# Performance work log

Hardware: AMD Instinct MI355X
Metric: run time of the kernel (lower is better)

The kernel has to match this reference:

```python
import jax, jax.numpy as jnp
import numpy as np


def gcn_conv(x, W, b, src, dst, n_nodes):
    """PyG-style GCNConv: x' = D^{-1/2}(A+I)D^{-1/2} X W + b, with self-loops added."""
    h = x @ W  # [N, F_out]
    # add self-loops
    loop = jnp.arange(n_nodes, dtype=src.dtype)
    s = jnp.concatenate([src, loop])  # [E+N]
    d = jnp.concatenate([dst, loop])  # [E+N]
    # symmetric normalization: deg counted over incoming edges (incl. self-loops)
    deg = jax.ops.segment_sum(jnp.ones_like(d, dtype=h.dtype), d, num_segments=n_nodes)
    dinv = jnp.where(deg > 0, jax.lax.rsqrt(deg), 0.0)
    coef = dinv[s] * dinv[d]  # [E+N]
    msg = h[s] * coef[:, None]  # gather + scale, [E+N, F_out]
    out = jax.ops.segment_sum(msg, d, num_segments=n_nodes)  # scatter-add
    return out + b


def setup_inputs() -> dict:
    key = jax.random.key(0)
    ks = jax.random.split(key, 6)
    N, E, F_IN, F_HID, F_OUT = 50000, 800000, 128, 128, 64
    x = jax.random.normal(ks[0], (N, F_IN), dtype=jnp.float32)
    edge_index = jax.random.randint(ks[1], (2, E), 0, N, dtype=jnp.int64)
    W0 = jax.random.normal(ks[2], (F_IN, F_HID), dtype=jnp.float32) * (F_IN ** -0.5)
    b0 = jnp.zeros((F_HID,), dtype=jnp.float32)
    W1 = jax.random.normal(ks[3], (F_HID, F_HID), dtype=jnp.float32) * (F_HID ** -0.5)
    b1 = jnp.zeros((F_HID,), dtype=jnp.float32)
    W2 = jax.random.normal(ks[4], (F_HID, F_OUT), dtype=jnp.float32) * (F_HID ** -0.5)
    b2 = jnp.zeros((F_OUT,), dtype=jnp.float32)
    return {"x": x, "edge_index": edge_index, "W0": W0, "b0": b0,
            "W1": W1, "b1": b1, "W2": W2, "b2": b2}


def reference(x, edge_index, W0, b0, W1, b1, W2, b2):
    n_nodes = x.shape[0]
    src, dst = edge_index[0], edge_index[1]
    # hidden GCNConv layers with relu (dropout is identity in eval mode)
    h = jax.nn.relu(gcn_conv(x, W0, b0, src, dst, n_nodes))
    h = jax.nn.relu(gcn_conv(h, W1, b1, src, dst, n_nodes))
    # final conv, no activation
    return gcn_conv(h, W2, b2, src, dst, n_nodes)
```

## Files before the change

### kernel.cpp

```cpp
#include <hip/hip_runtime.h>
#include <hip/hip_fp16.h>
#include <type_traits>

#define F_IN 128
#define NPART 8

typedef _Float16 f16x8 __attribute__((ext_vector_type(8)));
typedef _Float16 f16x4 __attribute__((ext_vector_type(4)));
typedef _Float16 f16x2 __attribute__((ext_vector_type(2)));
typedef float f32x4 __attribute__((ext_vector_type(4)));


__global__ void setup_kernel(const float* __restrict__ W0, const float* __restrict__ W1,
                             const float* __restrict__ W2, __half* __restrict__ Wt0,
                             __half* __restrict__ Wt1, __half* __restrict__ Wt2,
                             int* __restrict__ deg, int N) {
    int idx = blockIdx.x * 256 + threadIdx.x;
    if (idx < 16384) {
        int k = idx >> 7, n = idx & 127;
        Wt0[n * 128 + k] = __float2half_rn(W0[idx]);
    } else if (idx < 32768) {
        int j = idx - 16384;
        int k = j >> 7, n = j & 127;
        Wt1[n * 128 + k] = __float2half_rn(W1[j]);
    } else if (idx < 40960) {
        int j = idx - 32768;
        int k = j >> 6, n = j & 63;
        Wt2[n * 128 + k] = __float2half_rn(W2[j]);
    }
    if (idx < N) deg[idx] = 0;
}


__global__ __launch_bounds__(256) void deg_part_kernel(
    const int* __restrict__ dst, int* __restrict__ deg, int E, int psize)
{
    const int part  = blockIdx.x % NPART;
    const int bslot = blockIdx.x / NPART;
    const int nb    = gridDim.x / NPART;
    const int lo = part * psize;
    const int hi = lo + psize;
    for (int e = bslot * 256 + threadIdx.x; e < E; e += nb * 256) {
        int d = dst[e];
        if (d >= lo && d < hi) atomicAdd(&deg[d], 1);
    }
}


__global__ void scan_blocks(const int* __restrict__ deg, int* __restrict__ rp,
                            int* __restrict__ bsum, int N) {
    __shared__ int tmp[256];
    int t = threadIdx.x, i = blockIdx.x * 256 + t;
    int v = (i < N) ? deg[i] : 0;
    tmp[t] = v;
    __syncthreads();
    for (int off = 1; off < 256; off <<= 1) {
        int a = (t >= off) ? tmp[t - off] : 0;
        __syncthreads();
        tmp[t] += a;
        __syncthreads();
    }
    if (i < N) rp[i] = tmp[t] - v;
    if (t == 255) bsum[blockIdx.x] = tmp[255];
}

__global__ void add_offsets_kernel(int* __restrict__ rp, const int* __restrict__ bsum,
                                   int* __restrict__ cursor, const int* __restrict__ deg,
                                   float* __restrict__ dinv, int N, int nb) {
    __shared__ int tmp[256];
    int t = threadIdx.x;
    tmp[t] = (t < nb && t < (int)blockIdx.x) ? bsum[t] : 0;
    __syncthreads();
    for (int s = 128; s > 0; s >>= 1) {
        if (t < s) tmp[t] += tmp[t + s];
        __syncthreads();
    }
    int base = tmp[0];
    int i = blockIdx.x * 256 + t;
    if (i < N) {
        int r = rp[i] + base;
        rp[i] = r;
        cursor[i] = r;
        dinv[i] = rsqrtf((float)(deg[i] + 1));
    }
}

__global__ __launch_bounds__(256) void build_csr_kernel(
    const int* __restrict__ src, const int* __restrict__ dst,
    int* __restrict__ cursor, unsigned short* __restrict__ csr_src,
    int E, int psize)
{
    const int part  = blockIdx.x % NPART;
    const int bslot = blockIdx.x / NPART;
    const int nb    = gridDim.x / NPART;
    const int lo = part * psize;
    const int hi = lo + psize;
    for (int e = bslot * 256 + threadIdx.x; e < E; e += nb * 256) {
        int d = dst[e];
        if (d >= lo && d < hi) {
            int pos = atomicAdd(&cursor[d], 1);
            csr_src[pos] = (unsigned short)src[e];
        }
    }
}


template<int BN, typename XT>
__global__ __launch_bounds__(256) void gemm_mfma_kernel(
    const XT* __restrict__ X, const __half* __restrict__ Wt,
    const float* __restrict__ dinv, __half* __restrict__ g, int N)
{
    constexpr int K  = 128;
    constexpr int KP = K + 8;
    constexpr int NT = BN / 16;
    __shared__ __half Ws[BN * KP];

    const int tid = threadIdx.x;
    for (int c = tid; c < BN * (K / 8); c += 256) {
        int n  = c >> 4;
        int k8 = c & 15;
        *(f16x8*)&Ws[n * KP + k8 * 8] =
            *(const f16x8*)((const _Float16*)Wt + n * K + k8 * 8);
    }
    __syncthreads();

    const int lane = tid & 63;
    const int w    = tid >> 6;
    const int lrow = lane & 15;
    const int kg   = lane >> 4;
    const int row0 = blockIdx.x * 64 + w * 16;
    const int gr   = row0 + lrow;

    f32x4 acc[NT];
    #pragma unroll
    for (int t = 0; t < NT; ++t) acc[t] = (f32x4){0.f, 0.f, 0.f, 0.f};

    #pragma unroll
    for (int ks = 0; ks < 4; ++ks) {
        const int k0 = ks * 32 + kg * 8;
        f16x8 a = {};
        if constexpr (sizeof(XT) == 4) {
            if (gr < N) {
                const float* p = (const float*)X + (size_t)gr * K + k0;
                float4 x0 = *(const float4*)p;
                float4 x1 = *(const float4*)(p + 4);
                a[0] = (_Float16)x0.x; a[1] = (_Float16)x0.y;
                a[2] = (_Float16)x0.z; a[3] = (_Float16)x0.w;
                a[4] = (_Float16)x1.x; a[5] = (_Float16)x1.y;
                a[6] = (_Float16)x1.z; a[7] = (_Float16)x1.w;
            }
        } else {
            if (gr < N)
                a = *(const f16x8*)((const _Float16*)X + (size_t)gr * K + k0);
        }
        #pragma unroll
        for (int t = 0; t < NT; ++t) {
            f16x8 b = *(const f16x8*)&Ws[(t * 16 + lrow) * KP + k0];
            acc[t] = __builtin_amdgcn_mfma_f32_16x16x32_f16(a, b, acc[t], 0, 0, 0);
        }
    }

    #pragma unroll
    for (int r = 0; r < 4; ++r) {
        int m = row0 + kg * 4 + r;
        if (m < N) {
            float dn = dinv[m];
            #pragma unroll
            for (int t = 0; t < NT; ++t)
                g[(size_t)m * BN + t * 16 + lrow] = __float2half_rn(dn * acc[t][r]);
        }
    }
}


template<int FO, bool RELU, typename OT>
__global__ __launch_bounds__(256) void aggregate_kernel(
    const __half* __restrict__ g, const int* __restrict__ rp, const int* __restrict__ deg,
    const unsigned short* __restrict__ csr, const float* __restrict__ dinv,
    const float* __restrict__ bias, OT* __restrict__ out, int N)
{
    constexpr int PER = FO / 32;
    using VT = typename std::conditional<PER == 4, f16x4, f16x2>::type;

    int gid  = blockIdx.x * 256 + threadIdx.x;
    int node = gid >> 5;
    int lane = gid & 31;
    if (node >= N) return;

    int start = rp[node];
    int dg    = deg[node];

    const _Float16* gb = (const _Float16*)g + (size_t)lane * PER;

    float a[PER];
    {
        VT v = *(const VT*)(gb + (size_t)node * FO);
        #pragma unroll
        for (int p = 0; p < PER; ++p) a[p] = (float)v[p];
    }

    int j = 0;
    for (; j + 7 < dg; j += 8) {
        int s[8];
        #pragma unroll
        for (int q = 0; q < 8; ++q) s[q] = csr[start + j + q];
        VT v[8];
        #pragma unroll
        for (int q = 0; q < 8; ++q) v[q] = *(const VT*)(gb + (size_t)s[q] * FO);
        #pragma unroll
        for (int p = 0; p < PER; ++p)
            a[p] += (((float)v[0][p] + (float)v[1][p]) + ((float)v[2][p] + (float)v[3][p]))
                  + (((float)v[4][p] + (float)v[5][p]) + ((float)v[6][p] + (float)v[7][p]));
    }
    for (; j + 3 < dg; j += 4) {
        int s0 = csr[start + j];
        int s1 = csr[start + j + 1];
        int s2 = csr[start + j + 2];
        int s3 = csr[start + j + 3];
        VT v0 = *(const VT*)(gb + (size_t)s0 * FO);
        VT v1 = *(const VT*)(gb + (size_t)s1 * FO);
        VT v2 = *(const VT*)(gb + (size_t)s2 * FO);
        VT v3 = *(const VT*)(gb + (size_t)s3 * FO);
        #pragma unroll
        for (int p = 0; p < PER; ++p)
            a[p] += ((float)v0[p] + (float)v1[p]) + ((float)v2[p] + (float)v3[p]);
    }
    for (; j < dg; ++j) {
        int s0 = csr[start + j];
        VT v0 = *(const VT*)(gb + (size_t)s0 * FO);
        #pragma unroll
        for (int p = 0; p < PER; ++p) a[p] += (float)v0[p];
    }

    float dn = dinv[node];
    float o[PER];
    #pragma unroll
    for (int p = 0; p < PER; ++p) {
        o[p] = fmaf(dn, a[p], bias[lane * PER + p]);
        if (RELU) o[p] = fmaxf(o[p], 0.f);
    }

    if constexpr (sizeof(OT) == 2) {
        VT h;
        #pragma unroll
        for (int p = 0; p < PER; ++p) h[p] = (_Float16)o[p];
        *(VT*)((_Float16*)out + (size_t)node * FO + lane * PER) = h;
    } else {
        float* op = (float*)out + (size_t)node * FO + lane * PER;
        if constexpr (PER == 4) {
            *(float4*)op = make_float4(o[0], o[1], o[2], o[3]);
        } else {
            *(float2*)op = make_float2(o[0], o[1]);
        }
    }
}


extern "C" void kernel_launch(void* const* d_in, const int* in_sizes, int n_in,
                              void* d_out, int out_size, void* d_ws, size_t ws_size,
                              hipStream_t stream) {
    const float* x  = (const float*)d_in[0];
    const int*   ei = (const int*)d_in[1];
    const float* W0 = (const float*)d_in[2];
    const float* b0 = (const float*)d_in[3];
    const float* W1 = (const float*)d_in[4];
    const float* b1 = (const float*)d_in[5];
    const float* W2 = (const float*)d_in[6];
    const float* b2 = (const float*)d_in[7];
    float* out = (float*)d_out;

    const int N = in_sizes[0] / F_IN;
    const int E = in_sizes[1] / 2;
    const int* src = ei;
    const int* dst = ei + E;

    char* ws = (char*)d_ws;
    size_t off = 0;
    __half* bufA  = (__half*)(ws + off); off += (size_t)N * 128 * 2;
    __half* bufB  = (__half*)(ws + off); off += (size_t)N * 128 * 2;
    float* dinv   = (float*)(ws + off); off += (size_t)N * 4;
    int*   deg    = (int*)  (ws + off); off += (size_t)N * 4;
    int*   rowptr = (int*)  (ws + off); off += (size_t)N * 4;
    int*   cursor = (int*)  (ws + off); off += (size_t)N * 4;
    int*   bsum   = (int*)  (ws + off); off += 256 * 4;
    unsigned short* csr = (unsigned short*)(ws + off); off += (size_t)E * 2;
    off = (off + 255) & ~(size_t)255;
    __half* wt0 = (__half*)(ws + off); off += 128 * 128 * 2;
    __half* wt1 = (__half*)(ws + off); off += 128 * 128 * 2;
    __half* wt2 = (__half*)(ws + off); off += 64 * 128 * 2;

    const int nb_nodes = (N + 255) / 256;
    const int nb_setup = (((N > 40960 ? N : 40960) + 255) / 256);
    const int nb_aggr  = (N * 32 + 255) / 256;
    const int nb_gemm  = (N + 63) / 64;
    const int psize    = (N + NPART - 1) / NPART;

    setup_kernel<<<nb_setup, 256, 0, stream>>>(W0, W1, W2, wt0, wt1, wt2, deg, N);
    deg_part_kernel<<<NPART * 128, 256, 0, stream>>>(dst, deg, E, psize);
    scan_blocks<<<nb_nodes, 256, 0, stream>>>(deg, rowptr, bsum, N);
    add_offsets_kernel<<<nb_nodes, 256, 0, stream>>>(rowptr, bsum, cursor, deg, dinv, N, nb_nodes);
    build_csr_kernel<<<NPART * 128, 256, 0, stream>>>(src, dst, cursor, csr, E, psize);

    gemm_mfma_kernel<128, float><<<nb_gemm, 256, 0, stream>>>(x, wt0, dinv, bufA, N);
    aggregate_kernel<128, true, __half><<<nb_aggr, 256, 0, stream>>>(bufA, rowptr, deg, csr, dinv, b0, bufB, N);

    gemm_mfma_kernel<128, __half><<<nb_gemm, 256, 0, stream>>>(bufB, wt1, dinv, bufA, N);
    aggregate_kernel<128, true, __half><<<nb_aggr, 256, 0, stream>>>(bufA, rowptr, deg, csr, dinv, b1, bufB, N);

    gemm_mfma_kernel<64, __half><<<nb_gemm, 256, 0, stream>>>(bufB, wt2, dinv, bufA, N);
    aggregate_kernel<64, false, float><<<nb_aggr, 256, 0, stream>>>(bufA, rowptr, deg, csr, dinv, b2, out, N);
}
```

Measured before the change: 202.8 us.

## Slice aggregation features across XCDs so each XCD's L2 holds one feature slice

The aggregation kernel is restructured so each block handles a 32-feature slice for 32 nodes, with 8 threads per node. The block-to-XCD round-robin mapping (blockIdx & 7) is used so each XCD only ever gathers one feature slice, which shrinks the per-XCD working set of the gathered feature matrix and should raise L2 hit rates on the random neighbor gathers. The cost is that the CSR indices and row pointers are re-read once per slice, and each gather moves only 8 bytes per thread. Correctness relies on the grid being sized in multiples of 8, and the speed benefit relies on the hardware dispatching blocks round-robin across XCDs.

Result: slower. 215.1 us (+6.1%).

```diff
diff --git a/kernel.cpp b/kernel.cpp
--- a/kernel.cpp
+++ b/kernel.cpp
@@ -7,7 +7,6 @@
 
 typedef _Float16 f16x8 __attribute__((ext_vector_type(8)));
 typedef _Float16 f16x4 __attribute__((ext_vector_type(4)));
-typedef _Float16 f16x2 __attribute__((ext_vector_type(2)));
 typedef float f32x4 __attribute__((ext_vector_type(4)));
 
 
@@ -174,41 +173,46 @@
 
 
 template<int FO, bool RELU, typename OT>
-__global__ __launch_bounds__(256) void aggregate_kernel(
+__global__ __launch_bounds__(256) void aggregate_sliced_kernel(
     const __half* __restrict__ g, const int* __restrict__ rp, const int* __restrict__ deg,
     const unsigned short* __restrict__ csr, const float* __restrict__ dinv,
-    const float* __restrict__ bias, OT* __restrict__ out, int N)
+    const float* __restrict__ bias, OT* __restrict__ out, int N, int nbs)
 {
-    constexpr int PER = FO / 32;
-    using VT = typename std::conditional<PER == 4, f16x4, f16x2>::type;
-
-    int gid  = blockIdx.x * 256 + threadIdx.x;
-    int node = gid >> 5;
-    int lane = gid & 31;
+    constexpr int NSLICE = FO / 32;
+    constexpr int XPS    = 8 / NSLICE;
+
+    const int xcd   = blockIdx.x & 7;
+    const int slice = xcd / XPS;
+    const int nb_i  = (blockIdx.x >> 3) * XPS + (xcd % XPS);
+    if (nb_i >= nbs) return;
+
+    const int node = nb_i * 32 + (threadIdx.x >> 3);
+    const int l8   = threadIdx.x & 7;
     if (node >= N) return;
+
+    const int fbase = slice * 32 + l8 * 4;
+    const _Float16* gb = (const _Float16*)g + fbase;
+
+    float a[4];
+    {
+        f16x4 v = *(const f16x4*)(gb + (size_t)node * FO);
+        #pragma unroll
+        for (int p = 0; p < 4; ++p) a[p] = (float)v[p];
+    }
 
     int start = rp[node];
     int dg    = deg[node];
-
-    const _Float16* gb = (const _Float16*)g + (size_t)lane * PER;
-
-    float a[PER];
-    {
-        VT v = *(const VT*)(gb + (size_t)node * FO);
-        #pragma unroll
-        for (int p = 0; p < PER; ++p) a[p] = (float)v[p];
-    }
 
     int j = 0;
     for (; j + 7 < dg; j += 8) {
         int s[8];
         #pragma unroll
         for (int q = 0; q < 8; ++q) s[q] = csr[start + j + q];
-        VT v[8];
-        #pragma unroll
-        for (int q = 0; q < 8; ++q) v[q] = *(const VT*)(gb + (size_t)s[q] * FO);
-        #pragma unroll
-        for (int p = 0; p < PER; ++p)
+        f16x4 v[8];
+        #pragma unroll
+        for (int q = 0; q < 8; ++q) v[q] = *(const f16x4*)(gb + (size_t)s[q] * FO);
+        #pragma unroll
+        for (int p = 0; p < 4; ++p)
             a[p] += (((float)v[0][p] + (float)v[1][p]) + ((float)v[2][p] + (float)v[3][p]))
                   + (((float)v[4][p] + (float)v[5][p]) + ((float)v[6][p] + (float)v[7][p]));
     }
@@ -217,41 +221,37 @@
         int s1 = csr[start + j + 1];
         int s2 = csr[start + j + 2];
         int s3 = csr[start + j + 3];
-        VT v0 = *(const VT*)(gb + (size_t)s0 * FO);
-        VT v1 = *(const VT*)(gb + (size_t)s1 * FO);
-        VT v2 = *(const VT*)(gb + (size_t)s2 * FO);
-        VT v3 = *(const VT*)(gb + (size_t)s3 * FO);
-        #pragma unroll
-        for (int p = 0; p < PER; ++p)
+        f16x4 v0 = *(const f16x4*)(gb + (size_t)s0 * FO);
+        f16x4 v1 = *(const f16x4*)(gb + (size_t)s1 * FO);
+        f16x4 v2 = *(const f16x4*)(gb + (size_t)s2 * FO);
+        f16x4 v3 = *(const f16x4*)(gb + (size_t)s3 * FO);
+        #pragma unroll
+        for (int p = 0; p < 4; ++p)
             a[p] += ((float)v0[p] + (float)v1[p]) + ((float)v2[p] + (float)v3[p]);
     }
     for (; j < dg; ++j) {
         int s0 = csr[start + j];
-        VT v0 = *(const VT*)(gb + (size_t)s0 * FO);
-        #pragma unroll
-        for (int p = 0; p < PER; ++p) a[p] += (float)v0[p];
+        f16x4 v0 = *(const f16x4*)(gb + (size_t)s0 * FO);
+        #pragma unroll
+        for (int p = 0; p < 4; ++p) a[p] += (float)v0[p];
     }
 
     float dn = dinv[node];
-    float o[PER];
+    float o[4];
     #pragma unroll
-    for (int p = 0; p < PER; ++p) {
-        o[p] = fmaf(dn, a[p], bias[lane * PER + p]);
+    for (int p = 0; p < 4; ++p) {
+        o[p] = fmaf(dn, a[p], bias[fbase + p]);
         if (RELU) o[p] = fmaxf(o[p], 0.f);
     }
 
     if constexpr (sizeof(OT) == 2) {
-        VT h;
-        #pragma unroll
-        for (int p = 0; p < PER; ++p) h[p] = (_Float16)o[p];
-        *(VT*)((_Float16*)out + (size_t)node * FO + lane * PER) = h;
+        f16x4 h;
+        #pragma unroll
+        for (int p = 0; p < 4; ++p) h[p] = (_Float16)o[p];
+        *(f16x4*)((_Float16*)out + (size_t)node * FO + fbase) = h;
     } else {
-        float* op = (float*)out + (size_t)node * FO + lane * PER;
-        if constexpr (PER == 4) {
-            *(float4*)op = make_float4(o[0], o[1], o[2], o[3]);
-        } else {
-            *(float2*)op = make_float2(o[0], o[1]);
-        }
+        *(float4*)((float*)out + (size_t)node * FO + fbase) =
+            make_float4(o[0], o[1], o[2], o[3]);
     }
 }
 
@@ -291,9 +291,12 @@
 
     const int nb_nodes = (N + 255) / 256;
     const int nb_setup = (((N > 40960 ? N : 40960) + 255) / 256);
-    const int nb_aggr  = (N * 32 + 255) / 256;
     const int nb_gemm  = (N + 63) / 64;
     const int psize    = (N + NPART - 1) / NPART;
+
+    const int nbs      = (N + 31) / 32;
+    const int nb_ag128 = ((nbs + 1) / 2) * 8;
+    const int nb_ag64  = ((nbs + 3) / 4) * 8;
 
     setup_kernel<<<nb_setup, 256, 0, stream>>>(W0, W1, W2, wt0, wt1, wt2, deg, N);
     deg_part_kernel<<<NPART * 128, 256, 0, stream>>>(dst, deg, E, psize);
@@ -302,11 +305,11 @@
     build_csr_kernel<<<NPART * 128, 256, 0, stream>>>(src, dst, cursor, csr, E, psize);
 
     gemm_mfma_kernel<128, float><<<nb_gemm, 256, 0, stream>>>(x, wt0, dinv, bufA, N);
-    aggregate_kernel<128, true, __half><<<nb_aggr, 256, 0, stream>>>(bufA, rowptr, deg, csr, dinv, b0, bufB, N);
+    aggregate_sliced_kernel<128, true, __half><<<nb_ag128, 256, 0, stream>>>(bufA, rowptr, deg, csr, dinv, b0, bufB, N, nbs);
 
     gemm_mfma_kernel<128, __half><<<nb_gemm, 256, 0, stream>>>(bufB, wt1, dinv, bufA, N);
-    aggregate_kernel<128, true, __half><<<nb_aggr, 256, 0, stream>>>(bufA, rowptr, deg, csr, dinv, b1, bufB, N);
+    aggregate_sliced_kernel<128, true, __half><<<nb_ag128, 256, 0, stream>>>(bufA, rowptr, deg, csr, dinv, b1, bufB, N, nbs);
 
     gemm_mfma_kernel<64, __half><<<nb_gemm, 256, 0, stream>>>(bufB, wt2, dinv, bufA, N);
-    aggregate_kernel<64, false, float><<<nb_aggr, 256, 0, stream>>>(bufA, rowptr, deg, csr, dinv, b2, out, N);
-}
+    aggregate_sliced_kernel<64, false, float><<<nb_ag64, 256, 0, stream>>>(bufA, rowptr, deg, csr, dinv, b2, out, N, nbs);
+}
```
